# Kernel optimization log

Hardware: AMD Instinct MI355X
Metric: run time of the kernel (lower is better)

Reference implementation:

```python
import jax, jax.numpy as jnp
import numpy as np

C, N, E = 5, 50000, 800000   # relations (categories), nodes per category, edges per relation
DIN, H, DOUT = 128, 128, 64


def setup_inputs() -> dict:
    key = jax.random.key(0)
    ks = jax.random.split(key, 7)
    x = jax.random.normal(ks[0], (C, N, DIN), dtype=jnp.float32)
    edge_index = jax.random.randint(ks[1], (C, 2, E), 0, N)
    edge_weight = jax.random.uniform(ks[2], (C, E), dtype=jnp.float32, minval=0.1, maxval=1.0)
    W1 = jax.random.normal(ks[3], (C, DIN, H), dtype=jnp.float32) * (1.0 / np.sqrt(DIN))
    b1 = jnp.zeros((C, H), dtype=jnp.float32)
    W2 = jax.random.normal(ks[4], (C, H, DOUT), dtype=jnp.float32) * (1.0 / np.sqrt(H))
    b2 = jnp.zeros((C, DOUT), dtype=jnp.float32)
    return {"x": x, "edge_index": edge_index, "edge_weight": edge_weight,
            "W1": W1, "b1": b1, "W2": W2, "b2": b2}


def gcn_layer(x, src, dst, w, W, b):
    """PyG GCNConv: linear -> symmetric-normalized weighted scatter-add -> bias.
    Self-loops added with weight 1 (PyG default add_self_loops=True)."""
    n = x.shape[0]
    loop = jnp.arange(n)
    s = jnp.concatenate([src, loop])          # [E+N]
    d = jnp.concatenate([dst, loop])
    wa = jnp.concatenate([w, jnp.ones((n,), w.dtype)])
    deg = jax.ops.segment_sum(wa, d, num_segments=n)      # weighted in-degree (col)
    deg_safe = jnp.where(deg > 0, deg, 1.0)
    dis = jnp.where(deg > 0, jax.lax.rsqrt(deg_safe), 0.0)  # deg^-1/2, inf->0
    norm = dis[s] * wa * dis[d]                # [E+N]
    h = x @ W                                  # [N, F_out] transform before propagation
    msg = norm[:, None] * h[s]                 # gather + scale
    out = jnp.zeros((n, W.shape[1]), x.dtype).at[d].add(msg)  # scatter-add
    return out + b


def reference(x, edge_index, edge_weight, W1, b1, W2, b2):
    def per_relation(xc, ei, ew, w1, bb1, w2, bb2):
        h = jax.nn.relu(gcn_layer(xc, ei[0], ei[1], ew, w1, bb1))
        return gcn_layer(h, ei[0], ei[1], ew, w2, bb2)
    # Each node type receives from exactly one relation, so HeteroConv's 'sum'
    # aggregation is the identity; vmap over the 5 independent relations.
    return jax.vmap(per_relation)(x, edge_index, edge_weight, W1, b1, W2, b2)
```

## Files before the change

kernel.cpp:

```cpp
#include <hip/hip_runtime.h>
#include <hip/hip_fp16.h>

#define C_REL 5
#define NN    50000
#define EE    800000
#define D_IN  128
#define D_H   128
#define D_OUT 64

static constexpr int CN = C_REL * NN;
static constexpr int CE = C_REL * EE;
static constexpr int SCAN_B = (NN + 255) / 256;
static constexpr int BLK_GEMM_REL = (NN + 63) / 64;
static constexpr int BLK_AGG_REL  = NN / 4;
static constexpr int GEMM_BLOCKS  = C_REL * BLK_GEMM_REL;
static constexpr int HIST_BLOCKS  = 4096;
static constexpr int FUSED_GRID   = 2 * HIST_BLOCKS;
static constexpr int FILL0_BLOCKS = 1024;
static constexpr int AGGF_GRID    = 13750;
static constexpr int FILLS_BLOCKS = 1250;

static constexpr float FIX16     = 65536.0f;
static constexpr float FIX16_INV = 1.0f / 65536.0f;

__device__ inline unsigned pack2h(float a, float b) {
  __half2 h = __floats2half2_rn(a, b);
  return *reinterpret_cast<unsigned*>(&h);
}


__global__ __launch_bounds__(256) void init_kernel(unsigned* packed) {
  int i = blockIdx.x * 256 + threadIdx.x;
  if (i < CN) packed[i] = 0u;
}

__device__ inline void hist_body(int bid, int nblocks,
                                 const int* __restrict__ ei,
                                 const float* __restrict__ ew,
                                 unsigned* packed,
                                 int* __restrict__ pos) {
  int stride = nblocks * 256;
  for (int idx = bid * 256 + threadIdx.x; idx < CE; idx += stride) {
    int c = idx / EE, e = idx - c * EE;
    int d = ei[(c * 2 + 1) * EE + e];
    float w = ew[idx];
    unsigned wfix = (unsigned)(w * FIX16 + 0.5f);
    unsigned old = atomicAdd(&packed[c * NN + d], wfix | (1u << 22));
    pos[idx] = (int)(old >> 22);
  }
}

__global__ __launch_bounds__(256) void scan_a_kernel(const unsigned* __restrict__ packed,
                                                     int* rowptr, int* bsum,
                                                     float* __restrict__ dis) {
  int c = blockIdx.x / SCAN_B;
  int b = blockIdx.x - c * SCAN_B;
  int tid = threadIdx.x;
  int i = b * 256 + tid;
  int val = 0;
  if (i < NN) {
    unsigned p = packed[c * NN + i];
    val = (int)(p >> 22);
    dis[c * NN + i] = rsqrtf(1.0f + (float)(p & 0x3FFFFFu) * FIX16_INV);
  }
  __shared__ int sh[256];
  sh[tid] = val;
  __syncthreads();
  for (int off = 1; off < 256; off <<= 1) {
    int t = (tid >= off) ? sh[tid - off] : 0;
    __syncthreads();
    sh[tid] += t;
    __syncthreads();
  }
  if (i < NN) rowptr[c * (NN + 1) + i + 1] = sh[tid];
  if (tid == 255) bsum[c * 256 + b] = sh[255];
}

__global__ __launch_bounds__(256) void scan_c_kernel(int* rowptr, const int* __restrict__ bsum) {
  int c = blockIdx.x / SCAN_B;
  int b = blockIdx.x - c * SCAN_B;
  int tid = threadIdx.x;
  int lane = tid & 63;
  int acc = 0;
  for (int t = lane; t < b; t += 64) acc += bsum[c * 256 + t];
#pragma unroll
  for (int o = 1; o < 64; o <<= 1) acc += __shfl_xor(acc, o, 64);
  int i = b * 256 + tid;
  if (i < NN) rowptr[c * (NN + 1) + i + 1] += acc;
  if (i == 0) rowptr[c * (NN + 1)] = 0;
}

__device__ inline void fill_rel_body(int c, int bid, int nblocks,
                                     const int* __restrict__ ei,
                                     const float* __restrict__ ew,
                                     const float* __restrict__ dis,
                                     const int* __restrict__ rowptr,
                                     const int* __restrict__ pos,
                                     unsigned* __restrict__ csr) {
  int stride = nblocks * 256;
  const int* srcp = ei + (size_t)(c * 2) * EE;
  const int* dstp = srcp + EE;
  const float* ewc = ew + (size_t)c * EE;
  const int* posc = pos + (size_t)c * EE;
  const float* disc = dis + c * NN;
  const int* rpc = rowptr + c * (NN + 1);
  unsigned* csrc = csr + (size_t)c * EE;
  for (int e = bid * 256 + threadIdx.x; e < EE; e += stride) {
    int s = srcp[e];
    int d = dstp[e];
    float nrm = disc[s] * ewc[e] * disc[d];
    unsigned ent = (unsigned)s | ((unsigned)__half_as_ushort(__float2half_rn(nrm)) << 16);
    csrc[rpc[d] + posc[e]] = ent;
  }
}

__global__ __launch_bounds__(256) void fill0_kernel(const int* __restrict__ ei,
                                                    const float* __restrict__ ew,
                                                    const float* __restrict__ dis,
                                                    const int* __restrict__ rowptr,
                                                    const int* __restrict__ pos,
                                                    unsigned* __restrict__ csr) {
  fill_rel_body(0, blockIdx.x, FILL0_BLOCKS, ei, ew, dis, rowptr, pos, csr);
}


template <int NC, bool AHALF>
__device__ inline void gemm_body(int bid, const void* __restrict__ Av,
                                 const float* __restrict__ B,
                                 __half* __restrict__ Cout) {
  constexpr int K = 128;
  constexpr int KC = 32;
  constexpr int CPT = NC / 32;
  __shared__ float Bs[KC * NC];
  __shared__ float As[64][KC + 4];

  int c  = bid / BLK_GEMM_REL;
  int bl = bid - c * BLK_GEMM_REL;
  const float* Bc = B + (size_t)c * K * NC;
  __half* Cc = Cout + (size_t)c * NN * NC;

  int tid = threadIdx.x;
  int tx = tid & 31;
  int ty = tid >> 5;
  int rowBase = bl * 64;

  float acc[8][CPT];
#pragma unroll
  for (int i = 0; i < 8; ++i)
#pragma unroll
    for (int j = 0; j < CPT; ++j) acc[i][j] = 0.f;

  for (int kc = 0; kc < K; kc += KC) {
    __syncthreads();
    {
      const float4* B4 = (const float4*)(Bc + (size_t)kc * NC);
      float4* Bs4 = (float4*)Bs;
#pragma unroll
      for (int i = tid; i < KC * NC / 4; i += 256) Bs4[i] = B4[i];
    }
    if constexpr (AHALF) {
      const __half* Ac = (const __half*)Av + (size_t)c * NN * K;
      int lr = tid >> 2;
      int lc = (tid & 3) * 8;
      int gr = rowBase + lr;
      uint4 v = make_uint4(0u, 0u, 0u, 0u);
      if (gr < NN) v = *(const uint4*)&Ac[(size_t)gr * K + kc + lc];
      const __half2* hp = (const __half2*)&v;
#pragma unroll
      for (int j = 0; j < 4; ++j) {
        float2 f = __half22float2(hp[j]);
        As[lr][lc + 2 * j]     = f.x;
        As[lr][lc + 2 * j + 1] = f.y;
      }
    } else {
      const float* Ac = (const float*)Av + (size_t)c * NN * K;
      int lr = tid >> 3;
      int lc = (tid & 7) * 4;
#pragma unroll
      for (int rr = 0; rr < 64; rr += 32) {
        int r = lr + rr;
        int gr = rowBase + r;
        float4 v = make_float4(0.f, 0.f, 0.f, 0.f);
        if (gr < NN) v = *(const float4*)&Ac[(size_t)gr * K + kc + lc];
        *(float4*)&As[r][lc] = v;
      }
    }
    __syncthreads();

#pragma unroll
    for (int kk = 0; kk < KC; kk += 4) {
      float4 av[8];
#pragma unroll
      for (int i = 0; i < 8; ++i) av[i] = *(const float4*)&As[ty * 8 + i][kk];
#pragma unroll
      for (int u = 0; u < 4; ++u) {
        int k = kk + u;
        if constexpr (CPT == 4) {
          float4 bv = *(const float4*)&Bs[k * NC + tx * 4];
#pragma unroll
          for (int i = 0; i < 8; ++i) {
            float a = ((const float*)&av[i])[u];
            acc[i][0] += a * bv.x;
            acc[i][1] += a * bv.y;
            acc[i][2] += a * bv.z;
            acc[i][3] += a * bv.w;
          }
        } else {
          float2 bv = *(const float2*)&Bs[k * NC + tx * 2];
#pragma unroll
          for (int i = 0; i < 8; ++i) {
            float a = ((const float*)&av[i])[u];
            acc[i][0] += a * bv.x;
            acc[i][1] += a * bv.y;
          }
        }
      }
    }
  }

#pragma unroll
  for (int i = 0; i < 8; ++i) {
    int gr = rowBase + ty * 8 + i;
    if (gr >= NN) continue;
    if constexpr (CPT == 4) {
      unsigned lo = pack2h(acc[i][0], acc[i][1]);
      unsigned hi = pack2h(acc[i][2], acc[i][3]);
      *(uint2*)&Cc[(size_t)gr * NC + tx * 4] = make_uint2(lo, hi);
    } else {
      *(unsigned*)&Cc[(size_t)gr * NC + tx * 2] = pack2h(acc[i][0], acc[i][1]);
    }
  }
}

__global__ __launch_bounds__(256) void fused_hist_gemm1_kernel(
    const float* __restrict__ x, const float* __restrict__ W1, __half* __restrict__ h1,
    const int* __restrict__ ei, const float* __restrict__ ew,
    unsigned* packed, int* __restrict__ pos) {
  int id = blockIdx.x;
  if (id & 1) {
    hist_body(id >> 1, HIST_BLOCKS, ei, ew, packed, pos);
  } else {
    int gid = id >> 1;
    if (gid < GEMM_BLOCKS) gemm_body<D_H, false>(gid, x, W1, h1);
  }
}

__global__ __launch_bounds__(256) void gemm2_kernel(const __half* __restrict__ A,
                                                    const float* __restrict__ B,
                                                    __half* __restrict__ Cout) {
  gemm_body<D_OUT, true>(blockIdx.x, A, B, Cout);
}


__device__ inline void agg1_body(int bid, const __half2* __restrict__ h,
                                 const int* __restrict__ rowptr,
                                 const unsigned* __restrict__ csr,
                                 const float* __restrict__ dis,
                                 const float* __restrict__ bias,
                                 __half* __restrict__ out) {
  int c  = bid / BLK_AGG_REL;
  int bl = bid - c * BLK_AGG_REL;
  int node = bl * 4 + (threadIdx.x >> 6);
  int lane = threadIdx.x & 63;

  const __half2* hc = h + (size_t)c * (NN * 64);
  const unsigned* csrc = csr + (size_t)c * EE;
  int beg = __builtin_amdgcn_readfirstlane(rowptr[c * (NN + 1) + node]);
  int end = __builtin_amdgcn_readfirstlane(rowptr[c * (NN + 1) + node + 1]);

  float a0 = 0.f, a1 = 0.f;
#define AGG1_EDGE(ent)                                             \
  {                                                                \
    unsigned _e = (ent);                                           \
    unsigned _off = (_e & 0xffffu) * 64u + (unsigned)lane;         \
    float2 _v = __half22float2(hc[_off]);                          \
    float _nm = __half2float(__ushort_as_half((unsigned short)(_e >> 16))); \
    a0 += _nm * _v.x;                                              \
    a1 += _nm * _v.y;                                              \
  }
  int idx = beg;
  int hd = min(end, (beg + 3) & ~3);
  for (; idx < hd; ++idx) AGG1_EDGE(csrc[idx]);
  for (; idx + 4 <= end; idx += 4) {
    uint4 q = *(const uint4*)(csrc + idx);
    AGG1_EDGE(q.x);
    AGG1_EDGE(q.y);
    AGG1_EDGE(q.z);
    AGG1_EDGE(q.w);
  }
  for (; idx < end; ++idx) AGG1_EDGE(csrc[idx]);
#undef AGG1_EDGE

  float dn = dis[c * NN + node];
  float sn = dn * dn;
  float2 hv = __half22float2(hc[(unsigned)node * 64u + (unsigned)lane]);
  int f = lane * 2;
  a0 += sn * hv.x + bias[c * 128 + f];
  a1 += sn * hv.y + bias[c * 128 + f + 1];
  a0 = fmaxf(a0, 0.f);
  a1 = fmaxf(a1, 0.f);
  ((unsigned*)out)[((size_t)c * NN + node) * 64 + lane] = pack2h(a0, a1);
}

__global__ __launch_bounds__(256) void fused_agg1_fill_kernel(
    int c, const __half2* __restrict__ h, const int* __restrict__ rowptr,
    const unsigned* __restrict__ csr, const float* __restrict__ dis,
    const float* __restrict__ bias, __half* __restrict__ out,
    const int* __restrict__ ei, const float* __restrict__ ew,
    const int* __restrict__ pos) {
  int i = blockIdx.x;
  int r = i % 11;
  if (r < 10) {
    int aid = (i / 11) * 10 + r;
    agg1_body(c * BLK_AGG_REL + aid, h, rowptr, csr, dis, bias, out);
  } else if (c + 1 < C_REL) {
    fill_rel_body(c + 1, i / 11, FILLS_BLOCKS, ei, ew, dis, rowptr, pos,
                  (unsigned*)csr);
  }
}


__global__ __launch_bounds__(256) void agg2_kernel(const __half2* __restrict__ h,
                                                   const int* __restrict__ rowptr,
                                                   const unsigned* __restrict__ csr,
                                                   const float* __restrict__ dis,
                                                   const float* __restrict__ bias,
                                                   float* __restrict__ out) {
  int c  = blockIdx.x / BLK_AGG_REL;
  int bl = blockIdx.x - c * BLK_AGG_REL;
  int node = bl * 4 + (threadIdx.x >> 6);
  int lane = threadIdx.x & 63;
  int hf = lane >> 5;
  int fl = lane & 31;

  const __half2* hc = h + (size_t)c * (NN * 32);
  const unsigned* csrc = csr + (size_t)c * EE;
  int beg = __builtin_amdgcn_readfirstlane(rowptr[c * (NN + 1) + node]);
  int end = __builtin_amdgcn_readfirstlane(rowptr[c * (NN + 1) + node + 1]);

  float a0 = 0.f, a1 = 0.f;
  int idx = beg + hf;
  for (; idx + 2 < end; idx += 4) {
    unsigned ea = csrc[idx], eb = csrc[idx + 2];
    float2 va = __half22float2(hc[(ea & 0xffffu) * 32u + (unsigned)fl]);
    float2 vb = __half22float2(hc[(eb & 0xffffu) * 32u + (unsigned)fl]);
    float na = __half2float(__ushort_as_half((unsigned short)(ea >> 16)));
    float nb = __half2float(__ushort_as_half((unsigned short)(eb >> 16)));
    a0 += na * va.x + nb * vb.x;
    a1 += na * va.y + nb * vb.y;
  }
  for (; idx < end; idx += 2) {
    unsigned e = csrc[idx];
    float2 v = __half22float2(hc[(e & 0xffffu) * 32u + (unsigned)fl]);
    float nm = __half2float(__ushort_as_half((unsigned short)(e >> 16)));
    a0 += nm * v.x;
    a1 += nm * v.y;
  }
  a0 += __shfl_xor(a0, 32, 64);
  a1 += __shfl_xor(a1, 32, 64);
  if (hf == 0) {
    float dn = dis[c * NN + node];
    float sn = dn * dn;
    float2 hv = __half22float2(hc[(unsigned)node * 32u + (unsigned)fl]);
    int f = fl * 2;
    a0 += sn * hv.x + bias[c * 64 + f];
    a1 += sn * hv.y + bias[c * 64 + f + 1];
    *(float2*)&out[((size_t)c * NN + node) * 64 + f] = make_float2(a0, a1);
  }
}


extern "C" void kernel_launch(void* const* d_in, const int* in_sizes, int n_in,
                              void* d_out, int out_size, void* d_ws, size_t ws_size,
                              hipStream_t stream) {
  const float* x  = (const float*)d_in[0];
  const int*   ei = (const int*)d_in[1];
  const float* ew = (const float*)d_in[2];
  const float* W1 = (const float*)d_in[3];
  const float* b1 = (const float*)d_in[4];
  const float* W2 = (const float*)d_in[5];
  const float* b2 = (const float*)d_in[6];
  float* out = (float*)d_out;

  char* ws = (char*)d_ws;
  size_t off = 0;
  auto alloc = [&](size_t bytes) {
    size_t cur = off;
    off += (bytes + 255) & ~(size_t)255;
    return cur;
  };
  unsigned* packed = (unsigned*)(ws + alloc((size_t)CN * 4));
  float*    dis    = (float*)   (ws + alloc((size_t)CN * 4));
  int*      rowptr = (int*)     (ws + alloc((size_t)C_REL * (NN + 1) * 4));
  int*      bsum   = (int*)     (ws + alloc((size_t)C_REL * 256 * 4));
  unsigned* csr    = (unsigned*)(ws + alloc((size_t)CE * 4));
  __half*   h1     = (__half*)  (ws + alloc((size_t)CN * D_H * 2));
  __half*   agg1h  = (__half*)  (ws + alloc((size_t)CN * D_H * 2));
  int* pos = (int*)out;

  const int NB_CN = (CN + 255) / 256;

  init_kernel<<<NB_CN, 256, 0, stream>>>(packed);
  fused_hist_gemm1_kernel<<<FUSED_GRID, 256, 0, stream>>>(x, W1, h1, ei, ew, packed, pos);
  scan_a_kernel<<<C_REL * SCAN_B, 256, 0, stream>>>(packed, rowptr, bsum, dis);
  scan_c_kernel<<<C_REL * SCAN_B, 256, 0, stream>>>(rowptr, bsum);
  fill0_kernel<<<FILL0_BLOCKS, 256, 0, stream>>>(ei, ew, dis, rowptr, pos, csr);

  for (int c = 0; c < C_REL; ++c) {
    fused_agg1_fill_kernel<<<AGGF_GRID, 256, 0, stream>>>(
        c, (const __half2*)h1, rowptr, csr, dis, b1, agg1h, ei, ew, pos);
  }
  gemm2_kernel<<<C_REL * BLK_GEMM_REL, 256, 0, stream>>>(agg1h, W2, h1);
  agg2_kernel<<<C_REL * BLK_AGG_REL, 256, 0, stream>>>((const __half2*)h1, rowptr,
                                                       csr, dis, b2, out);
}
```

Baseline: 714.8 us.

## Bucket CSR neighbors by source range and process source ranges across node batches

The histogram now uses 64-bit packed counters holding four 10-bit per-source-range counts, so edges in each destination row are sub-bucketed by source quarter. The fill places edges accordingly. The aggregation kernels process 8 nodes per wave and sweep the source ranges in phase order, so gathers of the feature table stay within one quarter at a time and L2 locality improves. The fill and aggregation grid split are also retuned. The cost is wider atomics, an extra sub-boundary array, per-node loops that are no longer vectorized, and worse load balance across the 8 nodes in a wave.

```diff
diff --git a/kernel.cpp b/kernel.cpp
--- a/kernel.cpp
+++ b/kernel.cpp
@@ -12,13 +12,16 @@
 static constexpr int CE = C_REL * EE;
 static constexpr int SCAN_B = (NN + 255) / 256;
 static constexpr int BLK_GEMM_REL = (NN + 63) / 64;
-static constexpr int BLK_AGG_REL  = NN / 4;
 static constexpr int GEMM_BLOCKS  = C_REL * BLK_GEMM_REL;
 static constexpr int HIST_BLOCKS  = 4096;
 static constexpr int FUSED_GRID   = 2 * HIST_BLOCKS;
 static constexpr int FILL0_BLOCKS = 1024;
-static constexpr int AGGF_GRID    = 13750;
-static constexpr int FILLS_BLOCKS = 1250;
+
+static constexpr int RSZ  = 12500;
+static constexpr int NPW  = 8;
+static constexpr int A_BLOCKS  = 1568;
+static constexpr int AF_FILLB  = 448;
+static constexpr int AF_GRID   = A_BLOCKS + AF_FILLB;
 
 static constexpr float FIX16     = 65536.0f;
 static constexpr float FIX16_INV = 1.0f / 65536.0f;
@@ -29,39 +32,50 @@
 }
 
 
-__global__ __launch_bounds__(256) void init_kernel(unsigned* packed) {
+__global__ __launch_bounds__(256) void init_kernel(unsigned long long* packed) {
   int i = blockIdx.x * 256 + threadIdx.x;
-  if (i < CN) packed[i] = 0u;
+  if (i < CN) packed[i] = 0ULL;
 }
 
 __device__ inline void hist_body(int bid, int nblocks,
                                  const int* __restrict__ ei,
                                  const float* __restrict__ ew,
-                                 unsigned* packed,
+                                 unsigned long long* packed,
                                  int* __restrict__ pos) {
   int stride = nblocks * 256;
   for (int idx = bid * 256 + threadIdx.x; idx < CE; idx += stride) {
     int c = idx / EE, e = idx - c * EE;
+    int s = ei[(c * 2 + 0) * EE + e];
     int d = ei[(c * 2 + 1) * EE + e];
     float w = ew[idx];
     unsigned wfix = (unsigned)(w * FIX16 + 0.5f);
-    unsigned old = atomicAdd(&packed[c * NN + d], wfix | (1u << 22));
-    pos[idx] = (int)(old >> 22);
-  }
-}
-
-__global__ __launch_bounds__(256) void scan_a_kernel(const unsigned* __restrict__ packed,
+    int r = s / RSZ;
+    int sh = 24 + 10 * r;
+    unsigned long long old =
+        atomicAdd(&packed[c * NN + d], (unsigned long long)wfix | (1ULL << sh));
+    pos[idx] = (int)((old >> sh) & 1023ULL);
+  }
+}
+
+__global__ __launch_bounds__(256) void scan_a_kernel(const unsigned long long* __restrict__ packed,
                                                      int* rowptr, int* bsum,
-                                                     float* __restrict__ dis) {
+                                                     float* __restrict__ dis,
+                                                     uint2* __restrict__ subb) {
   int c = blockIdx.x / SCAN_B;
   int b = blockIdx.x - c * SCAN_B;
   int tid = threadIdx.x;
   int i = b * 256 + tid;
   int val = 0;
   if (i < NN) {
-    unsigned p = packed[c * NN + i];
-    val = (int)(p >> 22);
-    dis[c * NN + i] = rsqrtf(1.0f + (float)(p & 0x3FFFFFu) * FIX16_INV);
+    unsigned long long p = packed[c * NN + i];
+    unsigned c0 = (unsigned)(p >> 24) & 1023u;
+    unsigned c1 = (unsigned)(p >> 34) & 1023u;
+    unsigned c2 = (unsigned)(p >> 44) & 1023u;
+    unsigned c3 = (unsigned)(p >> 54) & 1023u;
+    val = (int)(c0 + c1 + c2 + c3);
+    dis[c * NN + i] = rsqrtf(1.0f + (float)(unsigned)(p & 0xFFFFFFu) * FIX16_INV);
+    unsigned s1 = c0, s2 = c0 + c1, s3 = c0 + c1 + c2;
+    subb[c * NN + i] = make_uint2(s1 | (s2 << 16), s3 | ((unsigned)val << 16));
   }
   __shared__ int sh[256];
   sh[tid] = val;
@@ -95,6 +109,7 @@
                                      const float* __restrict__ ew,
                                      const float* __restrict__ dis,
                                      const int* __restrict__ rowptr,
+                                     const uint2* __restrict__ subb,
                                      const int* __restrict__ pos,
                                      unsigned* __restrict__ csr) {
   int stride = nblocks * 256;
@@ -104,13 +119,20 @@
   const int* posc = pos + (size_t)c * EE;
   const float* disc = dis + c * NN;
   const int* rpc = rowptr + c * (NN + 1);
+  const uint2* sbc = subb + (size_t)c * NN;
   unsigned* csrc = csr + (size_t)c * EE;
   for (int e = bid * 256 + threadIdx.x; e < EE; e += stride) {
     int s = srcp[e];
     int d = dstp[e];
     float nrm = disc[s] * ewc[e] * disc[d];
-    unsigned ent = (unsigned)s | ((unsigned)__half_as_ushort(__float2half_rn(nrm)) << 16);
-    csrc[rpc[d] + posc[e]] = ent;
+    int r = s / RSZ;
+    uint2 sb = sbc[d];
+    unsigned base = (r == 0) ? 0u
+                  : (r == 1) ? (sb.x & 0xffffu)
+                  : (r == 2) ? (sb.x >> 16)
+                             : (sb.y & 0xffffu);
+    int slot = rpc[d] + (int)base + posc[e];
+    csrc[slot] = (unsigned)s | ((unsigned)__half_as_ushort(__float2half_rn(nrm)) << 16);
   }
 }
 
@@ -118,9 +140,10 @@
                                                     const float* __restrict__ ew,
                                                     const float* __restrict__ dis,
                                                     const int* __restrict__ rowptr,
+                                                    const uint2* __restrict__ subb,
                                                     const int* __restrict__ pos,
                                                     unsigned* __restrict__ csr) {
-  fill_rel_body(0, blockIdx.x, FILL0_BLOCKS, ei, ew, dis, rowptr, pos, csr);
+  fill_rel_body(0, blockIdx.x, FILL0_BLOCKS, ei, ew, dis, rowptr, subb, pos, csr);
 }
 
 
@@ -235,7 +258,7 @@
 __global__ __launch_bounds__(256) void fused_hist_gemm1_kernel(
     const float* __restrict__ x, const float* __restrict__ W1, __half* __restrict__ h1,
     const int* __restrict__ ei, const float* __restrict__ ew,
-    unsigned* packed, int* __restrict__ pos) {
+    unsigned long long* packed, int* __restrict__ pos) {
   int id = blockIdx.x;
   if (id & 1) {
     hist_body(id >> 1, HIST_BLOCKS, ei, ew, packed, pos);
@@ -252,120 +275,153 @@
 }
 
 
-__device__ inline void agg1_body(int bid, const __half2* __restrict__ h,
+__device__ inline void agg1_body(int c, int wid, const __half2* __restrict__ h,
                                  const int* __restrict__ rowptr,
+                                 const uint2* __restrict__ subb,
                                  const unsigned* __restrict__ csr,
                                  const float* __restrict__ dis,
                                  const float* __restrict__ bias,
                                  __half* __restrict__ out) {
-  int c  = bid / BLK_AGG_REL;
-  int bl = bid - c * BLK_AGG_REL;
-  int node = bl * 4 + (threadIdx.x >> 6);
+  int nbase = wid * NPW;
+  if (nbase >= NN) return;
   int lane = threadIdx.x & 63;
-
   const __half2* hc = h + (size_t)c * (NN * 64);
   const unsigned* csrc = csr + (size_t)c * EE;
-  int beg = __builtin_amdgcn_readfirstlane(rowptr[c * (NN + 1) + node]);
-  int end = __builtin_amdgcn_readfirstlane(rowptr[c * (NN + 1) + node + 1]);
-
-  float a0 = 0.f, a1 = 0.f;
-#define AGG1_EDGE(ent)                                             \
-  {                                                                \
-    unsigned _e = (ent);                                           \
-    unsigned _off = (_e & 0xffffu) * 64u + (unsigned)lane;         \
-    float2 _v = __half22float2(hc[_off]);                          \
-    float _nm = __half2float(__ushort_as_half((unsigned short)(_e >> 16))); \
-    a0 += _nm * _v.x;                                              \
-    a1 += _nm * _v.y;                                              \
-  }
-  int idx = beg;
-  int hd = min(end, (beg + 3) & ~3);
-  for (; idx < hd; ++idx) AGG1_EDGE(csrc[idx]);
-  for (; idx + 4 <= end; idx += 4) {
-    uint4 q = *(const uint4*)(csrc + idx);
-    AGG1_EDGE(q.x);
-    AGG1_EDGE(q.y);
-    AGG1_EDGE(q.z);
-    AGG1_EDGE(q.w);
-  }
-  for (; idx < end; ++idx) AGG1_EDGE(csrc[idx]);
-#undef AGG1_EDGE
-
-  float dn = dis[c * NN + node];
-  float sn = dn * dn;
-  float2 hv = __half22float2(hc[(unsigned)node * 64u + (unsigned)lane]);
-  int f = lane * 2;
-  a0 += sn * hv.x + bias[c * 128 + f];
-  a1 += sn * hv.y + bias[c * 128 + f + 1];
-  a0 = fmaxf(a0, 0.f);
-  a1 = fmaxf(a1, 0.f);
-  ((unsigned*)out)[((size_t)c * NN + node) * 64 + lane] = pack2h(a0, a1);
+  const int* rpc = rowptr + c * (NN + 1);
+  const uint2* sbc = subb + (size_t)c * NN;
+
+  float a0[NPW], a1[NPW];
+  int beg[NPW];
+  unsigned sbx[NPW], sby[NPW];
+#pragma unroll
+  for (int i = 0; i < NPW; ++i) {
+    a0[i] = 0.f; a1[i] = 0.f;
+    beg[i] = rpc[nbase + i];
+    uint2 t = sbc[nbase + i];
+    sbx[i] = t.x; sby[i] = t.y;
+  }
+#pragma unroll
+  for (int p = 0; p < 4; ++p) {
+#pragma unroll
+    for (int i = 0; i < NPW; ++i) {
+      unsigned lo = (p == 0) ? 0u
+                  : (p == 1) ? (sbx[i] & 0xffffu)
+                  : (p == 2) ? (sbx[i] >> 16)
+                             : (sby[i] & 0xffffu);
+      unsigned hi = (p == 0) ? (sbx[i] & 0xffffu)
+                  : (p == 1) ? (sbx[i] >> 16)
+                  : (p == 2) ? (sby[i] & 0xffffu)
+                             : (sby[i] >> 16);
+      int ib = beg[i] + (int)lo;
+      int ie = beg[i] + (int)hi;
+      for (int idx = ib; idx < ie; ++idx) {
+        unsigned e = csrc[idx];
+        float2 v = __half22float2(hc[(e & 0xffffu) * 64u + (unsigned)lane]);
+        float nm = __half2float(__ushort_as_half((unsigned short)(e >> 16)));
+        a0[i] += nm * v.x;
+        a1[i] += nm * v.y;
+      }
+    }
+  }
+#pragma unroll
+  for (int i = 0; i < NPW; ++i) {
+    int node = nbase + i;
+    float dn = dis[c * NN + node];
+    float sn = dn * dn;
+    float2 hv = __half22float2(hc[(unsigned)node * 64u + (unsigned)lane]);
+    int f = lane * 2;
+    float r0 = a0[i] + sn * hv.x + bias[c * 128 + f];
+    float r1 = a1[i] + sn * hv.y + bias[c * 128 + f + 1];
+    ((unsigned*)out)[((size_t)c * NN + node) * 64 + lane] =
+        pack2h(fmaxf(r0, 0.f), fmaxf(r1, 0.f));
+  }
 }
 
 __global__ __launch_bounds__(256) void fused_agg1_fill_kernel(
     int c, const __half2* __restrict__ h, const int* __restrict__ rowptr,
-    const unsigned* __restrict__ csr, const float* __restrict__ dis,
-    const float* __restrict__ bias, __half* __restrict__ out,
-    const int* __restrict__ ei, const float* __restrict__ ew,
-    const int* __restrict__ pos) {
-  int i = blockIdx.x;
-  int r = i % 11;
-  if (r < 10) {
-    int aid = (i / 11) * 10 + r;
-    agg1_body(c * BLK_AGG_REL + aid, h, rowptr, csr, dis, bias, out);
+    const uint2* __restrict__ subb, const unsigned* __restrict__ csr,
+    const float* __restrict__ dis, const float* __restrict__ bias,
+    __half* __restrict__ out, const int* __restrict__ ei,
+    const float* __restrict__ ew, const int* __restrict__ pos) {
+  int bid = blockIdx.x;
+  if (bid < A_BLOCKS) {
+    int wid = bid * 4 + (threadIdx.x >> 6);
+    agg1_body(c, wid, h, rowptr, subb, csr, dis, bias, out);
   } else if (c + 1 < C_REL) {
-    fill_rel_body(c + 1, i / 11, FILLS_BLOCKS, ei, ew, dis, rowptr, pos,
+    fill_rel_body(c + 1, bid - A_BLOCKS, AF_FILLB, ei, ew, dis, rowptr, subb, pos,
                   (unsigned*)csr);
   }
 }
-
 
 __global__ __launch_bounds__(256) void agg2_kernel(const __half2* __restrict__ h,
                                                    const int* __restrict__ rowptr,
+                                                   const uint2* __restrict__ subb,
                                                    const unsigned* __restrict__ csr,
                                                    const float* __restrict__ dis,
                                                    const float* __restrict__ bias,
                                                    float* __restrict__ out) {
-  int c  = blockIdx.x / BLK_AGG_REL;
-  int bl = blockIdx.x - c * BLK_AGG_REL;
-  int node = bl * 4 + (threadIdx.x >> 6);
+  int c = blockIdx.x / A_BLOCKS;
+  int bid = blockIdx.x - c * A_BLOCKS;
+  int wid = bid * 4 + (threadIdx.x >> 6);
+  int nbase = wid * NPW;
+  if (nbase >= NN) return;
   int lane = threadIdx.x & 63;
   int hf = lane >> 5;
   int fl = lane & 31;
-
   const __half2* hc = h + (size_t)c * (NN * 32);
   const unsigned* csrc = csr + (size_t)c * EE;
-  int beg = __builtin_amdgcn_readfirstlane(rowptr[c * (NN + 1) + node]);
-  int end = __builtin_amdgcn_readfirstlane(rowptr[c * (NN + 1) + node + 1]);
-
-  float a0 = 0.f, a1 = 0.f;
-  int idx = beg + hf;
-  for (; idx + 2 < end; idx += 4) {
-    unsigned ea = csrc[idx], eb = csrc[idx + 2];
-    float2 va = __half22float2(hc[(ea & 0xffffu) * 32u + (unsigned)fl]);
-    float2 vb = __half22float2(hc[(eb & 0xffffu) * 32u + (unsigned)fl]);
-    float na = __half2float(__ushort_as_half((unsigned short)(ea >> 16)));
-    float nb = __half2float(__ushort_as_half((unsigned short)(eb >> 16)));
-    a0 += na * va.x + nb * vb.x;
-    a1 += na * va.y + nb * vb.y;
-  }
-  for (; idx < end; idx += 2) {
-    unsigned e = csrc[idx];
-    float2 v = __half22float2(hc[(e & 0xffffu) * 32u + (unsigned)fl]);
-    float nm = __half2float(__ushort_as_half((unsigned short)(e >> 16)));
-    a0 += nm * v.x;
-    a1 += nm * v.y;
-  }
-  a0 += __shfl_xor(a0, 32, 64);
-  a1 += __shfl_xor(a1, 32, 64);
+  const int* rpc = rowptr + c * (NN + 1);
+  const uint2* sbc = subb + (size_t)c * NN;
+
+  float a0[NPW], a1[NPW];
+  int beg[NPW];
+  unsigned sbx[NPW], sby[NPW];
+#pragma unroll
+  for (int i = 0; i < NPW; ++i) {
+    a0[i] = 0.f; a1[i] = 0.f;
+    beg[i] = rpc[nbase + i];
+    uint2 t = sbc[nbase + i];
+    sbx[i] = t.x; sby[i] = t.y;
+  }
+#pragma unroll
+  for (int p = 0; p < 4; ++p) {
+#pragma unroll
+    for (int i = 0; i < NPW; ++i) {
+      unsigned lo = (p == 0) ? 0u
+                  : (p == 1) ? (sbx[i] & 0xffffu)
+                  : (p == 2) ? (sbx[i] >> 16)
+                             : (sby[i] & 0xffffu);
+      unsigned hi = (p == 0) ? (sbx[i] & 0xffffu)
+                  : (p == 1) ? (sbx[i] >> 16)
+                  : (p == 2) ? (sby[i] & 0xffffu)
+                             : (sby[i] >> 16);
+      int ie = beg[i] + (int)hi;
+      for (int idx = beg[i] + (int)lo + hf; idx < ie; idx += 2) {
+        unsigned e = csrc[idx];
+        float2 v = __half22float2(hc[(e & 0xffffu) * 32u + (unsigned)fl]);
+        float nm = __half2float(__ushort_as_half((unsigned short)(e >> 16)));
+        a0[i] += nm * v.x;
+        a1[i] += nm * v.y;
+      }
+    }
+  }
+#pragma unroll
+  for (int i = 0; i < NPW; ++i) {
+    a0[i] += __shfl_xor(a0[i], 32, 64);
+    a1[i] += __shfl_xor(a1[i], 32, 64);
+  }
   if (hf == 0) {
-    float dn = dis[c * NN + node];
-    float sn = dn * dn;
-    float2 hv = __half22float2(hc[(unsigned)node * 32u + (unsigned)fl]);
-    int f = fl * 2;
-    a0 += sn * hv.x + bias[c * 64 + f];
-    a1 += sn * hv.y + bias[c * 64 + f + 1];
-    *(float2*)&out[((size_t)c * NN + node) * 64 + f] = make_float2(a0, a1);
+#pragma unroll
+    for (int i = 0; i < NPW; ++i) {
+      int node = nbase + i;
+      float dn = dis[c * NN + node];
+      float sn = dn * dn;
+      float2 hv = __half22float2(hc[(unsigned)node * 32u + (unsigned)fl]);
+      int f = fl * 2;
+      float r0 = a0[i] + sn * hv.x + bias[c * 64 + f];
+      float r1 = a1[i] + sn * hv.y + bias[c * 64 + f + 1];
+      *(float2*)&out[((size_t)c * NN + node) * 64 + f] = make_float2(r0, r1);
+    }
   }
 }
 
@@ -389,10 +445,11 @@
     off += (bytes + 255) & ~(size_t)255;
     return cur;
   };
-  unsigned* packed = (unsigned*)(ws + alloc((size_t)CN * 4));
+  unsigned long long* packed = (unsigned long long*)(ws + alloc((size_t)CN * 8));
   float*    dis    = (float*)   (ws + alloc((size_t)CN * 4));
   int*      rowptr = (int*)     (ws + alloc((size_t)C_REL * (NN + 1) * 4));
   int*      bsum   = (int*)     (ws + alloc((size_t)C_REL * 256 * 4));
+  uint2*    subb   = (uint2*)   (ws + alloc((size_t)CN * 8));
   unsigned* csr    = (unsigned*)(ws + alloc((size_t)CE * 4));
   __half*   h1     = (__half*)  (ws + alloc((size_t)CN * D_H * 2));
   __half*   agg1h  = (__half*)  (ws + alloc((size_t)CN * D_H * 2));
@@ -402,15 +459,15 @@
 
   init_kernel<<<NB_CN, 256, 0, stream>>>(packed);
   fused_hist_gemm1_kernel<<<FUSED_GRID, 256, 0, stream>>>(x, W1, h1, ei, ew, packed, pos);
-  scan_a_kernel<<<C_REL * SCAN_B, 256, 0, stream>>>(packed, rowptr, bsum, dis);
+  scan_a_kernel<<<C_REL * SCAN_B, 256, 0, stream>>>(packed, rowptr, bsum, dis, subb);
   scan_c_kernel<<<C_REL * SCAN_B, 256, 0, stream>>>(rowptr, bsum);
-  fill0_kernel<<<FILL0_BLOCKS, 256, 0, stream>>>(ei, ew, dis, rowptr, pos, csr);
+  fill0_kernel<<<FILL0_BLOCKS, 256, 0, stream>>>(ei, ew, dis, rowptr, subb, pos, csr);
 
   for (int c = 0; c < C_REL; ++c) {
-    fused_agg1_fill_kernel<<<AGGF_GRID, 256, 0, stream>>>(
-        c, (const __half2*)h1, rowptr, csr, dis, b1, agg1h, ei, ew, pos);
-  }
-  gemm2_kernel<<<C_REL * BLK_GEMM_REL, 256, 0, stream>>>(agg1h, W2, h1);
-  agg2_kernel<<<C_REL * BLK_AGG_REL, 256, 0, stream>>>((const __half2*)h1, rowptr,
-                                                       csr, dis, b2, out);
-}
+    fused_agg1_fill_kernel<<<AF_GRID, 256, 0, stream>>>(
+        c, (const __half2*)h1, rowptr, subb, csr, dis, b1, agg1h, ei, ew, pos);
+  }
+  gemm2_kernel<<<GEMM_BLOCKS, 256, 0, stream>>>(agg1h, W2, h1);
+  agg2_kernel<<<C_REL * A_BLOCKS, 256, 0, stream>>>((const __half2*)h1, rowptr, subb,
+                                                    csr, dis, b2, out);
+}
```

Result: slower. 1.017 ms (+42.2%).

## Software-pipeline agg1, gemm2, agg2 and fill across relations in one fused kernel

Applied to the files above, without the earlier changes.

Replaces the per-relation agg1+fill launches and the separate gemm2 and agg2 kernels with seven launches of a single fused kernel. Launch cc runs agg1 for relation cc, gemm2 for relation cc-1, agg2 for relation cc-2 and the CSR fill for relation cc+1, so memory-bound gathers overlap with the GEMM and the tail of the dependency chain. The scatter position buffer moves from the output buffer into workspace, because the output is now written during the pipeline. The risks are more workspace use and more resource contention between stages that share a launch.

```diff
diff --git a/kernel.cpp b/kernel.cpp
--- a/kernel.cpp
+++ b/kernel.cpp
@@ -17,7 +17,8 @@
 static constexpr int HIST_BLOCKS  = 4096;
 static constexpr int FUSED_GRID   = 2 * HIST_BLOCKS;
 static constexpr int FILL0_BLOCKS = 1024;
-static constexpr int AGGF_GRID    = 13750;
+static constexpr int PIPE_GROUPS  = 1250;
+static constexpr int PIPE_GRID    = PIPE_GROUPS * 22;
 static constexpr int FILLS_BLOCKS = 1250;
 
 static constexpr float FIX16     = 65536.0f;
@@ -245,12 +246,6 @@
   }
 }
 
-__global__ __launch_bounds__(256) void gemm2_kernel(const __half* __restrict__ A,
-                                                    const float* __restrict__ B,
-                                                    __half* __restrict__ Cout) {
-  gemm_body<D_OUT, true>(blockIdx.x, A, B, Cout);
-}
-
 
 __device__ inline void agg1_body(int bid, const __half2* __restrict__ h,
                                  const int* __restrict__ rowptr,
@@ -302,32 +297,14 @@
   ((unsigned*)out)[((size_t)c * NN + node) * 64 + lane] = pack2h(a0, a1);
 }
 
-__global__ __launch_bounds__(256) void fused_agg1_fill_kernel(
-    int c, const __half2* __restrict__ h, const int* __restrict__ rowptr,
-    const unsigned* __restrict__ csr, const float* __restrict__ dis,
-    const float* __restrict__ bias, __half* __restrict__ out,
-    const int* __restrict__ ei, const float* __restrict__ ew,
-    const int* __restrict__ pos) {
-  int i = blockIdx.x;
-  int r = i % 11;
-  if (r < 10) {
-    int aid = (i / 11) * 10 + r;
-    agg1_body(c * BLK_AGG_REL + aid, h, rowptr, csr, dis, bias, out);
-  } else if (c + 1 < C_REL) {
-    fill_rel_body(c + 1, i / 11, FILLS_BLOCKS, ei, ew, dis, rowptr, pos,
-                  (unsigned*)csr);
-  }
-}
-
-
-__global__ __launch_bounds__(256) void agg2_kernel(const __half2* __restrict__ h,
-                                                   const int* __restrict__ rowptr,
-                                                   const unsigned* __restrict__ csr,
-                                                   const float* __restrict__ dis,
-                                                   const float* __restrict__ bias,
-                                                   float* __restrict__ out) {
-  int c  = blockIdx.x / BLK_AGG_REL;
-  int bl = blockIdx.x - c * BLK_AGG_REL;
+__device__ inline void agg2_body(int bid, const __half2* __restrict__ h,
+                                 const int* __restrict__ rowptr,
+                                 const unsigned* __restrict__ csr,
+                                 const float* __restrict__ dis,
+                                 const float* __restrict__ bias,
+                                 float* __restrict__ out) {
+  int c  = bid / BLK_AGG_REL;
+  int bl = bid - c * BLK_AGG_REL;
   int node = bl * 4 + (threadIdx.x >> 6);
   int lane = threadIdx.x & 63;
   int hf = lane >> 5;
@@ -366,6 +343,35 @@
     a0 += sn * hv.x + bias[c * 64 + f];
     a1 += sn * hv.y + bias[c * 64 + f + 1];
     *(float2*)&out[((size_t)c * NN + node) * 64 + f] = make_float2(a0, a1);
+  }
+}
+
+
+__global__ __launch_bounds__(256) void fused_pipe_kernel(
+    int cc, const __half2* __restrict__ h1, const int* __restrict__ rowptr,
+    const unsigned* __restrict__ csr, const float* __restrict__ dis,
+    const float* __restrict__ b1, __half* __restrict__ agg1h,
+    const float* __restrict__ W2, const float* __restrict__ b2,
+    float* __restrict__ out, const int* __restrict__ ei,
+    const float* __restrict__ ew, const int* __restrict__ pos) {
+  int i = blockIdx.x;
+  int grp = i / 22;
+  int r = i - grp * 22;
+  if (r < 10) {
+    if (cc < C_REL)
+      agg1_body(cc * BLK_AGG_REL + grp * 10 + r, h1, rowptr, csr, dis, b1, agg1h);
+  } else if (r < 20) {
+    if (cc >= 2)
+      agg2_body((cc - 2) * BLK_AGG_REL + grp * 10 + (r - 10), h1, rowptr, csr, dis,
+                b2, out);
+  } else if (r == 20) {
+    if (cc + 1 < C_REL)
+      fill_rel_body(cc + 1, grp, FILLS_BLOCKS, ei, ew, dis, rowptr, pos,
+                    (unsigned*)csr);
+  } else {
+    if (cc >= 1 && cc <= C_REL && grp < BLK_GEMM_REL)
+      gemm_body<D_OUT, true>((cc - 1) * BLK_GEMM_REL + grp, agg1h, W2,
+                             (__half*)h1);
   }
 }
 
@@ -396,7 +402,7 @@
   unsigned* csr    = (unsigned*)(ws + alloc((size_t)CE * 4));
   __half*   h1     = (__half*)  (ws + alloc((size_t)CN * D_H * 2));
   __half*   agg1h  = (__half*)  (ws + alloc((size_t)CN * D_H * 2));
-  int* pos = (int*)out;
+  int*      pos    = (int*)     (ws + alloc((size_t)CE * 4));
 
   const int NB_CN = (CN + 255) / 256;
 
@@ -406,11 +412,8 @@
   scan_c_kernel<<<C_REL * SCAN_B, 256, 0, stream>>>(rowptr, bsum);
   fill0_kernel<<<FILL0_BLOCKS, 256, 0, stream>>>(ei, ew, dis, rowptr, pos, csr);
 
-  for (int c = 0; c < C_REL; ++c) {
-    fused_agg1_fill_kernel<<<AGGF_GRID, 256, 0, stream>>>(
-        c, (const __half2*)h1, rowptr, csr, dis, b1, agg1h, ei, ew, pos);
-  }
-  gemm2_kernel<<<C_REL * BLK_GEMM_REL, 256, 0, stream>>>(agg1h, W2, h1);
-  agg2_kernel<<<C_REL * BLK_AGG_REL, 256, 0, stream>>>((const __half2*)h1, rowptr,
-                                                       csr, dis, b2, out);
-}
+  for (int cc = 0; cc <= 6; ++cc) {
+    fused_pipe_kernel<<<PIPE_GRID, 256, 0, stream>>>(
+        cc, (const __half2*)h1, rowptr, csr, dis, b1, agg1h, W2, b2, out, ei, ew, pos);
+  }
+}
```

After: 883.8 us. 23.6% more time.
